# Performance work log

Hardware: AMD Instinct MI355X
Metric: run time of the kernel (lower is better)

## Reference

```python
import jax, jax.numpy as jnp
import numpy as np

B, T, N_EMBD, HEAD_SIZE = 4, 4096, 32, 32


def setup_inputs() -> dict:
    key = jax.random.key(0)
    k1, k2, k3, k4 = jax.random.split(key, 4)
    x = jax.random.normal(k1, (B, T, N_EMBD), dtype=jnp.float32)
    Wq = jax.random.normal(k2, (HEAD_SIZE, N_EMBD), dtype=jnp.float32) * (N_EMBD ** -0.5)
    Wk = jax.random.normal(k3, (HEAD_SIZE, N_EMBD), dtype=jnp.float32) * (N_EMBD ** -0.5)
    Wv = jax.random.normal(k4, (HEAD_SIZE, N_EMBD), dtype=jnp.float32) * (N_EMBD ** -0.5)
    return {"x": x, "Wq": Wq, "Wk": Wk, "Wv": Wv}


def reference(x, Wq, Wk, Wv):
    # Linear(bias=False): y = x @ W.T  -> [B, T, head_size]
    q = jnp.einsum('btn,hn->bth', x, Wq)
    k = jnp.einsum('btn,hn->bth', x, Wk)
    v = jnp.einsum('btn,hn->bth', x, Wv)
    scale = q.shape[-1] ** -0.5
    # [B, T, T] attention scores
    wei = jnp.einsum('bth,bsh->bts', q, k) * scale
    # Faithful to source: tril the scores, then mask entries equal to 0
    tril = jnp.tril(wei)
    wei = jax.nn.softmax(jnp.where(tril == 0, -jnp.inf, tril), axis=-1)
    return jnp.einsum('bts,bsh->bth', wei, v)
```

## Files before the change

kernel.cpp:

```cpp
#include <hip/hip_runtime.h>
#include <cmath>

#define BB 4
#define TT 4096
#define NE 32
#define HS 32

#define IPB 576
#define MAXSP 8
#define SLOT 288
#define FNEG (-1.0e30f)
#define BIAS 6.0f
#define SC2  0.25506953149031156f

typedef unsigned int uint32;
typedef __fp16 half2v __attribute__((ext_vector_type(2)));
typedef __fp16 half4v __attribute__((ext_vector_type(4)));
typedef __fp16 half8v __attribute__((ext_vector_type(8)));
typedef float f32x4 __attribute__((ext_vector_type(4)));

__device__ __forceinline__ half2v u2h(uint32 u) {
    union { uint32 u; half2v h; } x; x.u = u; return x.h;
}

#if __has_builtin(__builtin_amdgcn_cvt_pkrtz)
__device__ __forceinline__ half2v pkf16(float a, float b) {
    return __builtin_amdgcn_cvt_pkrtz(a, b);
}
#else
__device__ __forceinline__ half2v pkf16(float a, float b) {
    half2v h; h.x = (__fp16)a; h.y = (__fp16)b; return h;
}
#endif

__global__ __launch_bounds__(256) void qkv_proj(
    const float* __restrict__ x,
    const float* __restrict__ Wq,
    const float* __restrict__ Wk,
    const float* __restrict__ Wv,
    __fp16* __restrict__ Qh, __fp16* __restrict__ Kh,
    __fp16* __restrict__ Vt8)
{
    __shared__ float Wt[3][NE][HS];
    #pragma unroll
    for (int i = threadIdx.x; i < 3 * NE * HS; i += 256) {
        int m   = i >> 10;
        int idx = i & 1023;
        int h   = idx >> 5;
        int d   = idx & 31;
        const float* Wm = (m == 0) ? Wq : (m == 1) ? Wk : Wv;
        Wt[m][d][h] = Wm[h * NE + d];
    }
    __syncthreads();

    int tid = blockIdx.x * 256 + threadIdx.x;
    int row = tid >> 5;
    int h   = tid & 31;
    const float4* xr4 = reinterpret_cast<const float4*>(x + (size_t)row * NE);
    float4 xv4[8];
    #pragma unroll
    for (int k = 0; k < 8; ++k) xv4[k] = xr4[k];
    const float* xv = (const float*)xv4;
    float aq = 0.f, ak = 0.f, av = 0.f;
    #pragma unroll
    for (int d = 0; d < NE; ++d) {
        aq = fmaf(xv[d], Wt[0][d][h], aq);
        ak = fmaf(xv[d], Wt[1][d][h], ak);
        av = fmaf(xv[d], Wt[2][d][h], av);
    }
    size_t o = (size_t)row * HS + h;
    Qh[o] = (__fp16)(aq * SC2);
    Kh[o] = (__fp16)ak;
    int b = row >> 12, t = row & (TT - 1);
    Vt8[((size_t)(b * (TT / 4) + (t >> 2)) * 16 + (h & 15)) * 8
        + (h >> 4) * 4 + (t & 3)] = (__fp16)av;
}

__global__ __launch_bounds__(256, 4) void attn_partial(
    const __fp16* __restrict__ Qh, const __fp16* __restrict__ Kh,
    const __fp16* __restrict__ Vt8, float* __restrict__ part)
{
    int wave = threadIdx.x >> 6;
    int lane = threadIdx.x & 63;
    int item = (BB * IPB - 1) - (blockIdx.x * 4 + wave);
    int b = item / IPB;
    int r = item - b * IPB;
    int g = (int)((sqrtf((float)(4 + 2 * r)) - 2.0f) * 0.25f);
    if (g < 0) g = 0;
    while (8 * (g + 1) * (g + 2) <= r) ++g;
    while (8 * g * (g + 1) > r) --g;
    int rr = r - 8 * g * (g + 1);
    int tq = rr / (g + 1);
    int tt = 16 * g + tq;
    int sp = rr - tq * (g + 1);
    int qt0 = tt * 32;
    int kbase = sp * 512;
    int kend  = min(kbase + 512, qt0 + 32);
    int nsub  = (kend - kbase) >> 4;
    bool hasdiag = (kend == qt0 + 32);
    int nfast = nsub - (hasdiag ? 2 : 0);

    int c = lane & 15;
    int q = lane >> 4;

    const __fp16* Qb = Qh  + (size_t)b * TT * HS;
    const __fp16* Kb = Kh  + (size_t)b * TT * HS;
    const __fp16* Vb = Vt8 + (size_t)b * (TT / 4) * 128;

    union U4H8  { uint4 u; half8v h; };
    union U4H44 { uint4 u; half4v h4[2]; };
    union H4    { half4v h4; half2v h2[2]; };
    union H4U4  { half2v h[4]; uint4 u; };

    U4H8 qf0; qf0.u = *(const uint4*)(Qb + (size_t)(qt0 + c) * HS + 8 * q);
    U4H8 qf1; qf1.u = *(const uint4*)(Qb + (size_t)(qt0 + 16 + c) * HS + 8 * q);

    const f32x4 cbias = {-BIAS, -BIAS, -BIAS, -BIAS};
    float l0 = 0.f, l1 = 0.f;
    f32x4 o00 = {0.f,0.f,0.f,0.f}, o01 = o00, o10 = o00, o11 = o00;

    auto dofast = [&](U4H8 kf, U4H44 vf) {
        f32x4 s0 = __builtin_amdgcn_mfma_f32_16x16x32_f16(kf.h, qf0.h, cbias, 0, 0, 0);
        f32x4 s1 = __builtin_amdgcn_mfma_f32_16x16x32_f16(kf.h, qf1.h, cbias, 0, 0, 0);
        float p0[4], p1[4];
        #pragma unroll
        for (int j = 0; j < 4; ++j) {
            p0[j] = exp2f((s0[j] != -BIAS) ? s0[j] : FNEG);
            p1[j] = exp2f((s1[j] != -BIAS) ? s1[j] : FNEG);
        }
        l0 += (p0[0] + p0[1]) + (p0[2] + p0[3]);
        l1 += (p1[0] + p1[1]) + (p1[2] + p1[3]);
        H4 pf0; pf0.h2[0] = pkf16(p0[0], p0[1]); pf0.h2[1] = pkf16(p0[2], p0[3]);
        H4 pf1; pf1.h2[0] = pkf16(p1[0], p1[1]); pf1.h2[1] = pkf16(p1[2], p1[3]);
        o00 = __builtin_amdgcn_mfma_f32_16x16x16f16(vf.h4[0], pf0.h4, o00, 0, 0, 0);
        o01 = __builtin_amdgcn_mfma_f32_16x16x16f16(vf.h4[1], pf0.h4, o01, 0, 0, 0);
        o10 = __builtin_amdgcn_mfma_f32_16x16x16f16(vf.h4[0], pf1.h4, o10, 0, 0, 0);
        o11 = __builtin_amdgcn_mfma_f32_16x16x16f16(vf.h4[1], pf1.h4, o11, 0, 0, 0);
    };

    auto domask = [&](int kb) {
        U4H8 kf; kf.u = *(const uint4*)(Kb + (size_t)(kb + c) * HS + 8 * q);
        U4H44 vf; vf.u = *(const uint4*)(Vb + (size_t)((kb >> 2) + q) * 128 + c * 8);
        f32x4 s0 = __builtin_amdgcn_mfma_f32_16x16x32_f16(kf.h, qf0.h, cbias, 0, 0, 0);
        f32x4 s1 = __builtin_amdgcn_mfma_f32_16x16x32_f16(kf.h, qf1.h, cbias, 0, 0, 0);
        int r0 = kb - qt0 + 4 * q;
        int r1 = r0 - 16;
        float p0[4], p1[4];
        #pragma unroll
        for (int j = 0; j < 4; ++j) {
            float w0 = (s0[j] != -BIAS) ? s0[j] : FNEG;
            float w1 = (s1[j] != -BIAS) ? s1[j] : FNEG;
            if (r0 + j > c) w0 = FNEG;
            if (r1 + j > c) w1 = FNEG;
            p0[j] = exp2f(w0);
            p1[j] = exp2f(w1);
        }
        l0 += (p0[0] + p0[1]) + (p0[2] + p0[3]);
        l1 += (p1[0] + p1[1]) + (p1[2] + p1[3]);
        H4 pf0; pf0.h2[0] = pkf16(p0[0], p0[1]); pf0.h2[1] = pkf16(p0[2], p0[3]);
        H4 pf1; pf1.h2[0] = pkf16(p1[0], p1[1]); pf1.h2[1] = pkf16(p1[2], p1[3]);
        o00 = __builtin_amdgcn_mfma_f32_16x16x16f16(vf.h4[0], pf0.h4, o00, 0, 0, 0);
        o01 = __builtin_amdgcn_mfma_f32_16x16x16f16(vf.h4[1], pf0.h4, o01, 0, 0, 0);
        o10 = __builtin_amdgcn_mfma_f32_16x16x16f16(vf.h4[0], pf1.h4, o10, 0, 0, 0);
        o11 = __builtin_amdgcn_mfma_f32_16x16x16f16(vf.h4[1], pf1.h4, o11, 0, 0, 0);
    };

    int kb = kbase;
    U4H8  kf; kf.u = *(const uint4*)(Kb + (size_t)(kb + c) * HS + 8 * q);
    U4H44 vf; vf.u = *(const uint4*)(Vb + (size_t)((kb >> 2) + q) * 128 + c * 8);
    #pragma unroll 2
    for (int i = 0; i < nfast; ++i) {
        int kb2 = kb + 16;
        U4H8  kf2; kf2.u = *(const uint4*)(Kb + (size_t)(kb2 + c) * HS + 8 * q);
        U4H44 vf2; vf2.u = *(const uint4*)(Vb + (size_t)((kb2 >> 2) + q) * 128 + c * 8);
        dofast(kf, vf);
        kf = kf2; vf = vf2; kb = kb2;
    }
    if (hasdiag) { domask(kb); domask(kb + 16); }

    float lt0 = l0 + __shfl_xor(l0, 16); lt0 += __shfl_xor(lt0, 32);
    float lt1 = l1 + __shfl_xor(l1, 16); lt1 += __shfl_xor(lt1, 32);

    float* P0 = part + (size_t)((b * 256 + 2 * tt) * MAXSP + sp) * SLOT;
    float* P1 = P0 + (size_t)MAXSP * SLOT;
    if (q == 0) { P0[16 + c] = lt0; P1[16 + c] = lt1; }
    H4U4 a;
    a.h[0] = pkf16(o00[0], o00[1]); a.h[1] = pkf16(o00[2], o00[3]);
    a.h[2] = pkf16(o01[0], o01[1]); a.h[3] = pkf16(o01[2], o01[3]);
    *((uint4*)((uint32*)(P0 + 32) + c * 16 + q * 4)) = a.u;
    a.h[0] = pkf16(o10[0], o10[1]); a.h[1] = pkf16(o10[2], o10[3]);
    a.h[2] = pkf16(o11[0], o11[1]); a.h[3] = pkf16(o11[2], o11[3]);
    *((uint4*)((uint32*)(P1 + 32) + c * 16 + q * 4)) = a.u;
}

__global__ __launch_bounds__(256) void attn_combine(
    const float* __restrict__ part, float* __restrict__ out)
{
    int tid = blockIdx.x * 256 + threadIdx.x;
    int hq = tid & 3;
    int c  = (tid >> 2) & 15;
    int t  = (tid >> 6) & 255;
    int b  = tid >> 14;
    int ns = (t >> 5) + 1;

    const float* base = part + (size_t)(b * 256 + t) * MAXSP * SLOT;

    float acc[8];
    #pragma unroll
    for (int k = 0; k < 8; ++k) acc[k] = 0.f;
    float L = 0.f;
    for (int s = 0; s < ns; ++s) {
        const float* P = base + (size_t)s * SLOT;
        L += P[16 + c];
        uint4 ov = *(const uint4*)((const uint32*)(P + 32) + c * 16 + 4 * hq);
        const uint32* ovp = (const uint32*)&ov;
        #pragma unroll
        for (int pr = 0; pr < 4; ++pr) {
            half2v hh = u2h(ovp[pr]);
            acc[2 * pr]     += (float)hh.x;
            acc[2 * pr + 1] += (float)hh.y;
        }
    }
    float invL = 1.0f / L;
    float* orow = out + ((size_t)(b * TT + t * 16 + c)) * HS;
    float4 w0 = {acc[0] * invL, acc[1] * invL, acc[2] * invL, acc[3] * invL};
    float4 w1 = {acc[4] * invL, acc[5] * invL, acc[6] * invL, acc[7] * invL};
    *(float4*)(orow + 4 * hq) = w0;
    *(float4*)(orow + 16 + 4 * hq) = w1;
}

extern "C" void kernel_launch(void* const* d_in, const int* in_sizes, int n_in,
                              void* d_out, int out_size, void* d_ws, size_t ws_size,
                              hipStream_t stream)
{
    const float* x  = (const float*)d_in[0];
    const float* Wq = (const float*)d_in[1];
    const float* Wk = (const float*)d_in[2];
    const float* Wv = (const float*)d_in[3];
    float* out = (float*)d_out;

    __fp16* Qh  = (__fp16*)d_ws;
    __fp16* Kh  = Qh + (size_t)BB * TT * HS;
    __fp16* Vt8 = Kh + (size_t)BB * TT * HS;
    float* part = (float*)(Vt8 + (size_t)BB * TT * HS);

    qkv_proj<<<dim3((BB * TT * HS) / 256), dim3(256), 0, stream>>>(
        x, Wq, Wk, Wv, Qh, Kh, Vt8);
    attn_partial<<<dim3((BB * IPB) / 4), dim3(256), 0, stream>>>(
        Qh, Kh, Vt8, part);
    attn_combine<<<dim3(256), dim3(256), 0, stream>>>(part, out);
}
```

Measured before the change: 105.7 us.

## Compute softmax row sums with MFMA against ones and deepen K/V prefetch

Replaces the scalar per-lane accumulation of softmax denominators and the cross-lane shuffle reduction with extra MFMA instructions that multiply the fp16 probabilities by a ones vector. This moves the adds onto the matrix unit and drops the final shuffles. It also deepens the K/V register prefetch from one tile ahead to two, reuses the prefetched tiles for the diagonal masked blocks, and raises the unroll factor. In exchange there are two more MFMAs per tile, the row sums are now built from fp16-rounded probabilities, and register pressure goes up.

```diff
diff --git a/kernel.cpp b/kernel.cpp
--- a/kernel.cpp
+++ b/kernel.cpp
@@ -116,8 +116,9 @@
     U4H8 qf1; qf1.u = *(const uint4*)(Qb + (size_t)(qt0 + 16 + c) * HS + 8 * q);
 
     const f32x4 cbias = {-BIAS, -BIAS, -BIAS, -BIAS};
-    float l0 = 0.f, l1 = 0.f;
+    const half4v vones = {(__fp16)1.0f, (__fp16)1.0f, (__fp16)1.0f, (__fp16)1.0f};
     f32x4 o00 = {0.f,0.f,0.f,0.f}, o01 = o00, o10 = o00, o11 = o00;
+    f32x4 al0 = o00, al1 = o00;
 
     auto dofast = [&](U4H8 kf, U4H44 vf) {
         f32x4 s0 = __builtin_amdgcn_mfma_f32_16x16x32_f16(kf.h, qf0.h, cbias, 0, 0, 0);
@@ -128,19 +129,17 @@
             p0[j] = exp2f((s0[j] != -BIAS) ? s0[j] : FNEG);
             p1[j] = exp2f((s1[j] != -BIAS) ? s1[j] : FNEG);
         }
-        l0 += (p0[0] + p0[1]) + (p0[2] + p0[3]);
-        l1 += (p1[0] + p1[1]) + (p1[2] + p1[3]);
         H4 pf0; pf0.h2[0] = pkf16(p0[0], p0[1]); pf0.h2[1] = pkf16(p0[2], p0[3]);
         H4 pf1; pf1.h2[0] = pkf16(p1[0], p1[1]); pf1.h2[1] = pkf16(p1[2], p1[3]);
+        al0 = __builtin_amdgcn_mfma_f32_16x16x16f16(vones,     pf0.h4, al0, 0, 0, 0);
+        al1 = __builtin_amdgcn_mfma_f32_16x16x16f16(vones,     pf1.h4, al1, 0, 0, 0);
         o00 = __builtin_amdgcn_mfma_f32_16x16x16f16(vf.h4[0], pf0.h4, o00, 0, 0, 0);
         o01 = __builtin_amdgcn_mfma_f32_16x16x16f16(vf.h4[1], pf0.h4, o01, 0, 0, 0);
         o10 = __builtin_amdgcn_mfma_f32_16x16x16f16(vf.h4[0], pf1.h4, o10, 0, 0, 0);
         o11 = __builtin_amdgcn_mfma_f32_16x16x16f16(vf.h4[1], pf1.h4, o11, 0, 0, 0);
     };
 
-    auto domask = [&](int kb) {
-        U4H8 kf; kf.u = *(const uint4*)(Kb + (size_t)(kb + c) * HS + 8 * q);
-        U4H44 vf; vf.u = *(const uint4*)(Vb + (size_t)((kb >> 2) + q) * 128 + c * 8);
+    auto domask = [&](U4H8 kf, U4H44 vf, int kb) {
         f32x4 s0 = __builtin_amdgcn_mfma_f32_16x16x32_f16(kf.h, qf0.h, cbias, 0, 0, 0);
         f32x4 s1 = __builtin_amdgcn_mfma_f32_16x16x32_f16(kf.h, qf1.h, cbias, 0, 0, 0);
         int r0 = kb - qt0 + 4 * q;
@@ -155,10 +154,10 @@
             p0[j] = exp2f(w0);
             p1[j] = exp2f(w1);
         }
-        l0 += (p0[0] + p0[1]) + (p0[2] + p0[3]);
-        l1 += (p1[0] + p1[1]) + (p1[2] + p1[3]);
         H4 pf0; pf0.h2[0] = pkf16(p0[0], p0[1]); pf0.h2[1] = pkf16(p0[2], p0[3]);
         H4 pf1; pf1.h2[0] = pkf16(p1[0], p1[1]); pf1.h2[1] = pkf16(p1[2], p1[3]);
+        al0 = __builtin_amdgcn_mfma_f32_16x16x16f16(vones,     pf0.h4, al0, 0, 0, 0);
+        al1 = __builtin_amdgcn_mfma_f32_16x16x16f16(vones,     pf1.h4, al1, 0, 0, 0);
         o00 = __builtin_amdgcn_mfma_f32_16x16x16f16(vf.h4[0], pf0.h4, o00, 0, 0, 0);
         o01 = __builtin_amdgcn_mfma_f32_16x16x16f16(vf.h4[1], pf0.h4, o01, 0, 0, 0);
         o10 = __builtin_amdgcn_mfma_f32_16x16x16f16(vf.h4[0], pf1.h4, o10, 0, 0, 0);
@@ -166,20 +165,24 @@
     };
 
     int kb = kbase;
-    U4H8  kf; kf.u = *(const uint4*)(Kb + (size_t)(kb + c) * HS + 8 * q);
-    U4H44 vf; vf.u = *(const uint4*)(Vb + (size_t)((kb >> 2) + q) * 128 + c * 8);
-    #pragma unroll 2
+    U4H8  kfa, kfb; U4H44 vfa, vfb;
+    kfa.u = *(const uint4*)(Kb + (size_t)(kb + c) * HS + 8 * q);
+    vfa.u = *(const uint4*)(Vb + (size_t)((kb >> 2) + q) * 128 + c * 8);
+    kfb.u = *(const uint4*)(Kb + (size_t)(kb + 16 + c) * HS + 8 * q);
+    vfb.u = *(const uint4*)(Vb + (size_t)(((kb + 16) >> 2) + q) * 128 + c * 8);
+    #pragma unroll 4
     for (int i = 0; i < nfast; ++i) {
-        int kb2 = kb + 16;
-        U4H8  kf2; kf2.u = *(const uint4*)(Kb + (size_t)(kb2 + c) * HS + 8 * q);
-        U4H44 vf2; vf2.u = *(const uint4*)(Vb + (size_t)((kb2 >> 2) + q) * 128 + c * 8);
-        dofast(kf, vf);
-        kf = kf2; vf = vf2; kb = kb2;
-    }
-    if (hasdiag) { domask(kb); domask(kb + 16); }
-
-    float lt0 = l0 + __shfl_xor(l0, 16); lt0 += __shfl_xor(lt0, 32);
-    float lt1 = l1 + __shfl_xor(l1, 16); lt1 += __shfl_xor(lt1, 32);
+        int kb2 = kb + 32;
+        U4H8  kfc; kfc.u = *(const uint4*)(Kb + (size_t)(kb2 + c) * HS + 8 * q);
+        U4H44 vfc; vfc.u = *(const uint4*)(Vb + (size_t)((kb2 >> 2) + q) * 128 + c * 8);
+        dofast(kfa, vfa);
+        kfa = kfb; vfa = vfb; kfb = kfc; vfb = vfc;
+        kb += 16;
+    }
+    if (hasdiag) { domask(kfa, vfa, kb); domask(kfb, vfb, kb + 16); }
+
+    float lt0 = al0[0];
+    float lt1 = al1[0];
 
     float* P0 = part + (size_t)((b * 256 + 2 * tt) * MAXSP + sp) * SLOT;
     float* P1 = P0 + (size_t)MAXSP * SLOT;
```

Measured after the change: 105.9 us. No clear change (+0.2%).
